# Kernel optimization log

Measured on AMD Instinct MI355X. Metric: run time of the kernel, lower is better.

## Reference

```python
import jax, jax.numpy as jnp
import numpy as np


def setup_inputs() -> dict:
    key = jax.random.key(0)
    ks = jax.random.split(key, 6)
    B, T, I, H, O = 64, 512, 256, 512, 256
    stdv = 1.0 / np.sqrt(H)
    u = lambda k, shape: jax.random.uniform(k, shape, jnp.float32, -stdv, stdv)
    return {
        "x": jax.random.normal(ks[0], (B, T, I), jnp.float32),
        "W": u(ks[1], (I, 4 * H)),
        "U": u(ks[2], (H, 4 * H)),
        "bias": u(ks[3], (4 * H,)),
        "Wl": u(ks[4], (H, O)),
        "bl": u(ks[5], (O,)),
    }


def lstm_scan(x, W, U, bias):
    B, T, I = x.shape
    H = U.shape[0]
    # Precompute input projections for all timesteps in one big GEMM: [B,T,4H]
    x_proj = jnp.einsum("bti,ig->btg", x, W) + bias

    def step(carry, xp_t):
        h, c = carry
        gates = xp_t + h @ U  # [B, 4H]
        i_t = jax.nn.sigmoid(gates[:, :H])
        f_t = jax.nn.sigmoid(gates[:, H:2 * H])
        g_t = jnp.tanh(gates[:, 2 * H:3 * H])
        o_t = jax.nn.sigmoid(gates[:, 3 * H:])
        c_new = f_t * c + i_t * g_t
        h_new = o_t * jnp.tanh(c_new)
        return (h_new, c_new), h_new

    h0 = jnp.zeros((B, H), x.dtype)
    c0 = jnp.zeros((B, H), x.dtype)
    (h_T, c_T), hs = jax.lax.scan(step, (h0, c0), jnp.swapaxes(x_proj, 0, 1))
    hidden_seq = jnp.swapaxes(hs, 0, 1)  # [B, T, H]
    return hidden_seq, h_T, c_T


def reference(x, W, U, bias, Wl, bl):
    hidden_seq, h_T, c_T = lstm_scan(x, W, U, bias)
    out = hidden_seq @ Wl + bl  # [B, T, O]
    return out, (h_T, c_T)
```

## Files before the change

### kernel.cpp

```cpp
#include <hip/hip_runtime.h>
#include <stdint.h>

typedef uint16_t u16;
typedef uint32_t u32;
typedef unsigned long long u64;
typedef __attribute__((ext_vector_type(8))) __bf16 bf16x8;
typedef __attribute__((ext_vector_type(8))) short short8;
typedef __attribute__((ext_vector_type(4))) float floatx4;

__device__ __forceinline__ float bf2f(u16 u) {
  union { u32 i; float f; } v; v.i = ((u32)u) << 16; return v.f;
}
__device__ __forceinline__ u16 f2bf(float f) {
  union { float f; u32 i; } v; v.f = f;
  u32 i = v.i;
  return (u16)((i + 0x7FFFu + ((i >> 16) & 1u)) >> 16);
}
__device__ __forceinline__ float sigm(float x) { return 1.f / (1.f + __expf(-x)); }
__device__ __forceinline__ float tanh_f(float x) {
  x = fminf(15.f, fmaxf(-15.f, x));
  float e = __expf(2.f * x);
  return (e - 1.f) / (e + 1.f);
}

__global__ void transpose_f32_bf16(const float* __restrict__ src, u16* __restrict__ dst,
                                   int R, int C) {
  __shared__ u16 tile[32][33];
  int x = blockIdx.x * 32 + threadIdx.x;
#pragma unroll
  for (int j = 0; j < 4; ++j) {
    int y = blockIdx.y * 32 + threadIdx.y + j * 8;
    if (x < C && y < R) tile[threadIdx.y + j * 8][threadIdx.x] = f2bf(src[(size_t)y * C + x]);
  }
  __syncthreads();
  int x2 = blockIdx.y * 32 + threadIdx.x;
#pragma unroll
  for (int j = 0; j < 4; ++j) {
    int y2 = blockIdx.x * 32 + threadIdx.y + j * 8;
    if (x2 < R && y2 < C) dst[(size_t)y2 * R + x2] = tile[threadIdx.x][threadIdx.y + j * 8];
  }
}

__global__ __launch_bounds__(256) void gemm_a32_bt(
    const float* __restrict__ A, const u16* __restrict__ BT,
    const float* __restrict__ bias, u16* __restrict__ C,
    int M, int N, int K) {
  __shared__ __align__(16) u16 As[64 * 40];
  __shared__ __align__(16) u16 Bs[64 * 40];
  const int tid = threadIdx.x;
  const int wave = tid >> 6, lane = tid & 63;
  const int q4 = lane >> 4, n16 = lane & 15;
  const int mw = (wave >> 1) * 32, nw = (wave & 1) * 32;
  const int m0 = blockIdx.y * 64, n0 = blockIdx.x * 64;
  const int ldrow = tid >> 2, ldseg = (tid & 3) * 8;

  floatx4 acc[2][2] = {};
  for (int k0 = 0; k0 < K; k0 += 32) {
    const float* ap = A + (size_t)(m0 + ldrow) * K + k0 + ldseg;
    floatx4 a0 = *(const floatx4*)ap;
    floatx4 a1 = *(const floatx4*)(ap + 4);
    short8 s;
    s[0] = (short)f2bf(a0[0]); s[1] = (short)f2bf(a0[1]);
    s[2] = (short)f2bf(a0[2]); s[3] = (short)f2bf(a0[3]);
    s[4] = (short)f2bf(a1[0]); s[5] = (short)f2bf(a1[1]);
    s[6] = (short)f2bf(a1[2]); s[7] = (short)f2bf(a1[3]);
    *(short8*)(As + ldrow * 40 + ldseg) = s;
    *(short8*)(Bs + ldrow * 40 + ldseg) =
        *(const short8*)(BT + (size_t)(n0 + ldrow) * K + k0 + ldseg);
    __syncthreads();
#pragma unroll
    for (int mi = 0; mi < 2; ++mi) {
      bf16x8 a = *(const bf16x8*)(As + (mw + mi * 16 + n16) * 40 + q4 * 8);
#pragma unroll
      for (int ni = 0; ni < 2; ++ni) {
        bf16x8 b = *(const bf16x8*)(Bs + (nw + ni * 16 + n16) * 40 + q4 * 8);
        acc[mi][ni] = __builtin_amdgcn_mfma_f32_16x16x32_bf16(a, b, acc[mi][ni], 0, 0, 0);
      }
    }
    __syncthreads();
  }
#pragma unroll
  for (int mi = 0; mi < 2; ++mi)
#pragma unroll
    for (int ni = 0; ni < 2; ++ni) {
      int col = n0 + nw + ni * 16 + n16;
      float bv = bias[col];
#pragma unroll
      for (int r = 0; r < 4; ++r) {
        int m = m0 + mw + mi * 16 + q4 * 4 + r;
        C[(size_t)m * N + col] = f2bf(acc[mi][ni][r] + bv);
      }
    }
}

__global__ __launch_bounds__(256) void gemm_bt_f32out_perm(
    const u16* __restrict__ A, const u16* __restrict__ BT,
    const float* __restrict__ bias, float* __restrict__ C,
    int M, int N, int K) {
  __shared__ __align__(16) u16 As[64 * 40];
  __shared__ __align__(16) u16 Bs[64 * 40];
  const int tid = threadIdx.x;
  const int wave = tid >> 6, lane = tid & 63;
  const int q4 = lane >> 4, n16 = lane & 15;
  const int mw = (wave >> 1) * 32, nw = (wave & 1) * 32;
  const int m0 = blockIdx.y * 64, n0 = blockIdx.x * 64;
  const int ldrow = tid >> 2, ldseg = (tid & 3) * 8;

  const int mm = m0 + ldrow;
  const size_t slot = ((size_t)((mm >> 13) * 512 + ((mm & 8191) >> 4))) * 8192
                      + (mm & 15) * 16;

  floatx4 acc[2][2] = {};
  for (int k0 = 0; k0 < K; k0 += 32) {
    int kk = k0 + ldseg;
    *(short8*)(As + ldrow * 40 + ldseg) =
        *(const short8*)(A + slot + (kk >> 4) * 256 + (kk & 15));
    *(short8*)(Bs + ldrow * 40 + ldseg) =
        *(const short8*)(BT + (size_t)(n0 + ldrow) * K + k0 + ldseg);
    __syncthreads();
#pragma unroll
    for (int mi = 0; mi < 2; ++mi) {
      bf16x8 a = *(const bf16x8*)(As + (mw + mi * 16 + n16) * 40 + q4 * 8);
#pragma unroll
      for (int ni = 0; ni < 2; ++ni) {
        bf16x8 b = *(const bf16x8*)(Bs + (nw + ni * 16 + n16) * 40 + q4 * 8);
        acc[mi][ni] = __builtin_amdgcn_mfma_f32_16x16x32_bf16(a, b, acc[mi][ni], 0, 0, 0);
      }
    }
    __syncthreads();
  }
#pragma unroll
  for (int mi = 0; mi < 2; ++mi)
#pragma unroll
    for (int ni = 0; ni < 2; ++ni) {
      int col = n0 + nw + ni * 16 + n16;
      float bv = bias[col];
#pragma unroll
      for (int r = 0; r < 4; ++r) {
        int m = m0 + mw + mi * 16 + q4 * 4 + r;
        int orow = ((m >> 13) * 16 + (m & 15)) * 512 + ((m & 8191) >> 4);
        C[(size_t)orow * N + col] = acc[mi][ni][r] + bv;
      }
    }
}

#define T_STEPS 512
#define HLSZ (16 * 520)
__global__ __launch_bounds__(256, 1) void lstm_scan(
    const u16* __restrict__ xp,
    const u16* __restrict__ UT,
    u16* __restrict__ hT_all,
    float* __restrict__ out_hT,
    float* __restrict__ out_cT) {
  const int bi = blockIdx.x;
  const int g = (bi & 7) >> 1;
  const int wgi = ((bi & 1) << 2) | (bi >> 3);
  const int tid = threadIdx.x;
  const int wave = tid >> 6;
  const int lane = tid & 63;
  const int n = lane & 15;
  const int q4 = lane >> 4;
  const int cb = wgi * 64 + wave * 16;
  const int p = wgi * 4 + wave;

  __shared__ __align__(16) u16 hls[2 * HLSZ];
  __shared__ __align__(8) u16 hstw[4 * 256];
  u16* hp = hstw + wave * 256;

  bf16x8 u[4][16];
#pragma unroll
  for (int qg = 0; qg < 4; ++qg) {
    const u16* up = UT + (size_t)(qg * 512 + cb + n) * 512;
#pragma unroll
    for (int kt = 0; kt < 16; ++kt)
      u[qg][kt] = *(const bf16x8*)(up + kt * 32 + q4 * 8);
  }

  float cst[4] = {0.f, 0.f, 0.f, 0.f};
  const u16* xp_base = xp + (size_t)(g * 16) * T_STEPS * 2048;

#pragma unroll 1
  for (int t = 0; t < T_STEPS; ++t) {
    float xpv[4][4];
#pragma unroll
    for (int qg = 0; qg < 4; ++qg)
#pragma unroll
      for (int r = 0; r < 4; ++r)
        xpv[qg][r] = bf2f(xp_base[((size_t)(q4 * 4 + r) * T_STEPS + t) * 2048
                                  + qg * 512 + cb + n]);
    __asm__ volatile("" ::: "memory");

    floatx4 acc[4] = {};
    if (t > 0) {
      const u64* hsrc = (const u64*)(hT_all) + (size_t)(g * T_STEPS + (t - 1)) * 2048;
      u64 v[8];
      for (;;) {
#pragma unroll
        for (int it = 0; it < 8; ++it)
          v[it] = __hip_atomic_load(hsrc + it * 256 + tid,
                                    __ATOMIC_RELAXED, __HIP_MEMORY_SCOPE_AGENT);
        bool ok = true;
#pragma unroll
        for (int it = 0; it < 8; ++it) ok &= (v[it] != ~0ull);
        if (ok) break;
      }
      __asm__ volatile("" ::: "memory");

      u16* buf = hls + ((t - 1) & 1) * HLSZ;
#pragma unroll
      for (int it = 0; it < 8; ++it) {
        int idx = it * 256 + tid;
        int tile = idx >> 6, w = idx & 63;
        *(u64*)(buf + (w >> 2) * 520 + tile * 16 + (w & 3) * 4) = v[it];
      }
      __syncthreads();
#pragma unroll
      for (int kt = 0; kt < 16; ++kt) {
        bf16x8 a = *(const bf16x8*)(buf + n * 520 + kt * 32 + q4 * 8);
        acc[0] = __builtin_amdgcn_mfma_f32_16x16x32_bf16(a, u[0][kt], acc[0], 0, 0, 0);
        acc[1] = __builtin_amdgcn_mfma_f32_16x16x32_bf16(a, u[1][kt], acc[1], 0, 0, 0);
        acc[2] = __builtin_amdgcn_mfma_f32_16x16x32_bf16(a, u[2][kt], acc[2], 0, 0, 0);
        acc[3] = __builtin_amdgcn_mfma_f32_16x16x32_bf16(a, u[3][kt], acc[3], 0, 0, 0);
      }
    }

#pragma unroll
    for (int r = 0; r < 4; ++r) {
      float gi = sigm(acc[0][r] + xpv[0][r]);
      float gf = sigm(acc[1][r] + xpv[1][r]);
      float gg = tanh_f(acc[2][r] + xpv[2][r]);
      float go = sigm(acc[3][r] + xpv[3][r]);
      float cn = gf * cst[r] + gi * gg;
      cst[r] = cn;
      float hv = go * tanh_f(cn);
      int row = q4 * 4 + r;
      hp[row * 16 + n] = f2bf(hv);
      if (t == T_STEPS - 1) {
        out_hT[(g * 16 + row) * 512 + cb + n] = hv;
        out_cT[(g * 16 + row) * 512 + cb + n] = cn;
      }
    }
    __asm__ volatile("s_waitcnt lgkmcnt(0)" ::: "memory");

    {
      u64 v = *(const u64*)(hp + (lane >> 2) * 16 + (lane & 3) * 4);
      u64* hdst = (u64*)(hT_all) + (size_t)(g * T_STEPS + t) * 2048 + p * 64 + lane;
      __hip_atomic_store(hdst, v, __ATOMIC_RELAXED, __HIP_MEMORY_SCOPE_AGENT);
    }
  }
}

extern "C" void kernel_launch(void* const* d_in, const int* in_sizes, int n_in,
                              void* d_out, int out_size, void* d_ws, size_t ws_size,
                              hipStream_t stream) {
  (void)in_sizes; (void)n_in; (void)out_size; (void)ws_size;
  const float* x    = (const float*)d_in[0];
  const float* W    = (const float*)d_in[1];
  const float* U    = (const float*)d_in[2];
  const float* bias = (const float*)d_in[3];
  const float* Wl   = (const float*)d_in[4];
  const float* bl   = (const float*)d_in[5];
  float* out = (float*)d_out;
  char* ws = (char*)d_ws;

  u16* xp     = (u16*)(ws + 0);
  u16* UT     = (u16*)(ws + 134217728);
  u16* WT     = (u16*)(ws + 136314880);
  u16* WlT    = (u16*)(ws + 137363456);
  u16* hT_all = (u16*)(ws + 137625600);

  hipMemsetAsync(hT_all, 0xFF, 33554432, stream);

  transpose_f32_bf16<<<dim3(2048 / 32, 256 / 32), dim3(32, 8), 0, stream>>>(W, WT, 256, 2048);
  transpose_f32_bf16<<<dim3(2048 / 32, 512 / 32), dim3(32, 8), 0, stream>>>(U, UT, 512, 2048);
  transpose_f32_bf16<<<dim3(256 / 32, 512 / 32), dim3(32, 8), 0, stream>>>(Wl, WlT, 512, 256);

  gemm_a32_bt<<<dim3(2048 / 64, 32768 / 64), 256, 0, stream>>>(x, WT, bias, xp, 32768, 2048, 256);

  lstm_scan<<<32, 256, 0, stream>>>(xp, UT, hT_all,
                                    out + 8388608, out + 8421376);

  gemm_bt_f32out_perm<<<dim3(256 / 64, 32768 / 64), 256, 0, stream>>>(
      hT_all, WlT, bl, out, 32768, 256, 512);
}
```

Measured before the change: 1.483 ms.

## Poll hidden state directly into MFMA fragments with XCD-aware block placement

The scan kernel now launches 64 blocks and keeps only those whose block index maps to g<4. Each surviving block records its XCC id so the kernel can detect whether all 8 workgroups of a batch group landed on the same XCD. When they did, it polls the previous hidden state with buffer loads using sc0 (intended to hit the shared L2) directly into per-lane MFMA A fragments, skipping the LDS staging and __syncthreads. Otherwise it falls back to device-scope atomic loads. Stores are issued twice (plain plus atomic), and the first 512 bytes of the output are borrowed as scratch for the id exchange before the final GEMM overwrites them.

```diff
diff --git a/kernel.cpp b/kernel.cpp
--- a/kernel.cpp
+++ b/kernel.cpp
@@ -7,6 +7,8 @@
 typedef __attribute__((ext_vector_type(8))) __bf16 bf16x8;
 typedef __attribute__((ext_vector_type(8))) short short8;
 typedef __attribute__((ext_vector_type(4))) float floatx4;
+typedef __attribute__((ext_vector_type(2))) u64 u64x2;
+typedef __attribute__((ext_vector_type(4))) u32 u32x4;
 
 __device__ __forceinline__ float bf2f(u16 u) {
   union { u32 i; float f; } v; v.i = ((u32)u) << 16; return v.f;
@@ -145,16 +147,17 @@
 }
 
 #define T_STEPS 512
-#define HLSZ (16 * 520)
 __global__ __launch_bounds__(256, 1) void lstm_scan(
     const u16* __restrict__ xp,
     const u16* __restrict__ UT,
     u16* __restrict__ hT_all,
     float* __restrict__ out_hT,
-    float* __restrict__ out_cT) {
+    float* __restrict__ out_cT,
+    u64* __restrict__ ids) {
   const int bi = blockIdx.x;
-  const int g = (bi & 7) >> 1;
-  const int wgi = ((bi & 1) << 2) | (bi >> 3);
+  const int g = bi & 7;
+  if (g >= 4) return;
+  const int wgi = bi >> 3;
   const int tid = threadIdx.x;
   const int wave = tid >> 6;
   const int lane = tid & 63;
@@ -163,9 +166,41 @@
   const int cb = wgi * 64 + wave * 16;
   const int p = wgi * 4 + wave;
 
-  __shared__ __align__(16) u16 hls[2 * HLSZ];
   __shared__ __align__(8) u16 hstw[4 * 256];
+  __shared__ int s_mode;
   u16* hp = hstw + wave * 256;
+
+  if (tid == 0) {
+    u32 xcc = ((u32)__builtin_amdgcn_s_getreg(63508)) & 0xFu;
+    __hip_atomic_store(ids + g * 8 + wgi, (u64)(xcc + 1),
+                       __ATOMIC_RELAXED, __HIP_MEMORY_SCOPE_AGENT);
+    u64 v[8]; bool done = false;
+    for (int it = 0; it < 20000 && !done; ++it) {
+      done = true;
+#pragma unroll
+      for (int j = 0; j < 8; ++j) {
+        v[j] = __hip_atomic_load(ids + g * 8 + j,
+                                 __ATOMIC_RELAXED, __HIP_MEMORY_SCOPE_AGENT);
+        done &= (v[j] != 0ull);
+      }
+    }
+    bool same = done;
+    if (done) {
+#pragma unroll
+      for (int j = 1; j < 8; ++j) same &= (v[j] == v[0]);
+    }
+    s_mode = same ? 0 : 1;
+  }
+  __syncthreads();
+  int mode = s_mode;
+  int fails = 0;
+
+  u32x4 srsrc;
+  {
+    u64 a = (u64)(uintptr_t)hT_all;
+    srsrc.x = (u32)a; srsrc.y = (u32)(a >> 32);
+    srsrc.z = 33554432u; srsrc.w = 0x00020000u;
+  }
 
   bf16x8 u[4][16];
 #pragma unroll
@@ -178,6 +213,7 @@
 
   float cst[4] = {0.f, 0.f, 0.f, 0.f};
   const u16* xp_base = xp + (size_t)(g * 16) * T_STEPS * 2048;
+  const u32 fragoff = (u32)((q4 >> 1) * 256 + n * 16 + (q4 & 1) * 8);
 
 #pragma unroll 1
   for (int t = 0; t < T_STEPS; ++t) {
@@ -192,31 +228,61 @@
 
     floatx4 acc[4] = {};
     if (t > 0) {
-      const u64* hsrc = (const u64*)(hT_all) + (size_t)(g * T_STEPS + (t - 1)) * 2048;
-      u64 v[8];
-      for (;;) {
-#pragma unroll
-        for (int it = 0; it < 8; ++it)
-          v[it] = __hip_atomic_load(hsrc + it * 256 + tid,
-                                    __ATOMIC_RELAXED, __HIP_MEMORY_SCOPE_AGENT);
-        bool ok = true;
-#pragma unroll
-        for (int it = 0; it < 8; ++it) ok &= (v[it] != ~0ull);
-        if (ok) break;
+      const u32 frag_u16 = (u32)(g * T_STEPS + (t - 1)) * 8192u + fragoff;
+      u64x2 f[16];
+      bool have = false;
+
+      if (mode == 0) {
+        int sweeps = 0;
+        for (;;) {
+#pragma unroll
+          for (int kt = 0; kt < 16; ++kt)
+            asm volatile("buffer_load_dwordx4 %0, %1, %2, 0 offen sc0"
+                         : "=&v"(f[kt])
+                         : "v"((frag_u16 + (u32)kt * 512u) * 2u), "s"(srsrc));
+          asm volatile("s_waitcnt vmcnt(0)" ::: "memory");
+          __builtin_amdgcn_sched_barrier(0);
+#pragma unroll
+          for (int kt = 0; kt < 16; ++kt)
+            asm volatile("" : "+v"(f[kt]));
+          bool ok = true;
+#pragma unroll
+          for (int kt = 0; kt < 16; ++kt)
+            ok = ok & (f[kt][0] != ~0ull) & (f[kt][1] != ~0ull);
+          if (__all((int)ok)) { have = true; break; }
+          if (++sweeps > 1024) {
+            if (++fails >= 3) mode = 1;
+            break;
+          }
+        }
+      }
+      if (!have) {
+        const u64* hb = (const u64*)hT_all + (size_t)(frag_u16 >> 2);
+        for (;;) {
+          u64 lo[16], hi[16];
+#pragma unroll
+          for (int kt = 0; kt < 16; ++kt) {
+            lo[kt] = __hip_atomic_load(hb + kt * 128,
+                                       __ATOMIC_RELAXED, __HIP_MEMORY_SCOPE_AGENT);
+            hi[kt] = __hip_atomic_load(hb + kt * 128 + 1,
+                                       __ATOMIC_RELAXED, __HIP_MEMORY_SCOPE_AGENT);
+          }
+          bool ok = true;
+#pragma unroll
+          for (int kt = 0; kt < 16; ++kt)
+            ok = ok & (lo[kt] != ~0ull) & (hi[kt] != ~0ull);
+          if (__all((int)ok)) {
+#pragma unroll
+            for (int kt = 0; kt < 16; ++kt) { f[kt][0] = lo[kt]; f[kt][1] = hi[kt]; }
+            break;
+          }
+        }
       }
       __asm__ volatile("" ::: "memory");
 
-      u16* buf = hls + ((t - 1) & 1) * HLSZ;
-#pragma unroll
-      for (int it = 0; it < 8; ++it) {
-        int idx = it * 256 + tid;
-        int tile = idx >> 6, w = idx & 63;
-        *(u64*)(buf + (w >> 2) * 520 + tile * 16 + (w & 3) * 4) = v[it];
-      }
-      __syncthreads();
 #pragma unroll
       for (int kt = 0; kt < 16; ++kt) {
-        bf16x8 a = *(const bf16x8*)(buf + n * 520 + kt * 32 + q4 * 8);
+        bf16x8 a = __builtin_bit_cast(bf16x8, f[kt]);
         acc[0] = __builtin_amdgcn_mfma_f32_16x16x32_bf16(a, u[0][kt], acc[0], 0, 0, 0);
         acc[1] = __builtin_amdgcn_mfma_f32_16x16x32_bf16(a, u[1][kt], acc[1], 0, 0, 0);
         acc[2] = __builtin_amdgcn_mfma_f32_16x16x32_bf16(a, u[2][kt], acc[2], 0, 0, 0);
@@ -245,6 +311,7 @@
     {
       u64 v = *(const u64*)(hp + (lane >> 2) * 16 + (lane & 3) * 4);
       u64* hdst = (u64*)(hT_all) + (size_t)(g * T_STEPS + t) * 2048 + p * 64 + lane;
+      asm volatile("global_store_dwordx2 %0, %1, off" :: "v"(hdst), "v"(v) : "memory");
       __hip_atomic_store(hdst, v, __ATOMIC_RELAXED, __HIP_MEMORY_SCOPE_AGENT);
     }
   }
@@ -270,6 +337,7 @@
   u16* hT_all = (u16*)(ws + 137625600);
 
   hipMemsetAsync(hT_all, 0xFF, 33554432, stream);
+  hipMemsetAsync(out, 0x00, 512, stream);
 
   transpose_f32_bf16<<<dim3(2048 / 32, 256 / 32), dim3(32, 8), 0, stream>>>(W, WT, 256, 2048);
   transpose_f32_bf16<<<dim3(2048 / 32, 512 / 32), dim3(32, 8), 0, stream>>>(U, UT, 512, 2048);
@@ -277,8 +345,8 @@
 
   gemm_a32_bt<<<dim3(2048 / 64, 32768 / 64), 256, 0, stream>>>(x, WT, bias, xp, 32768, 2048, 256);
 
-  lstm_scan<<<32, 256, 0, stream>>>(xp, UT, hT_all,
-                                    out + 8388608, out + 8421376);
+  lstm_scan<<<64, 256, 0, stream>>>(xp, UT, hT_all,
+                                    out + 8388608, out + 8421376, (u64*)out);
 
   gemm_bt_f32out_perm<<<dim3(256 / 64, 32768 / 64), 256, 0, stream>>>(
       hT_all, WlT, bl, out, 32768, 256, 512);
```

Result: slower. 4.511 ms (+204.1%).
